# Performance work log

Hardware: AMD Instinct MI355X
Metric: run time of the kernel (lower is better)

Reference implementation:

```python
import jax, jax.numpy as jnp
import numpy as np

N_NODES = 100000
N_REL = 3
N_EDGES = 1600000
IN_F, HID_F, N_CLS = 256, 128, 2


def setup_inputs() -> dict:
    key = jax.random.key(0)
    ks = jax.random.split(key, 6)
    x = jax.random.normal(ks[0], (N_NODES, IN_F), dtype=jnp.float32)
    # edges[r, 0] = src node ids, edges[r, 1] = dst node ids for relation r
    edges = jax.random.randint(ks[1], (N_REL, 2, N_EDGES), 0, N_NODES, dtype=jnp.int64)
    W1 = jax.random.normal(ks[2], (N_REL, IN_F, HID_F), dtype=jnp.float32) * 0.05
    b1 = jnp.zeros((N_REL, HID_F), dtype=jnp.float32)
    W2 = jax.random.normal(ks[3], (N_REL, HID_F, N_CLS), dtype=jnp.float32) * 0.05
    b2 = jnp.zeros((N_REL, N_CLS), dtype=jnp.float32)
    return {"x": x, "edges": edges, "W1": W1, "b1": b1, "W2": W2, "b2": b2}


def _hetero_graphconv(h, edges, W, b, n_nodes):
    """Sum over relations of DGL GraphConv(norm='both', bias=True).
    in_feats > out_feats for every layer here, so (as in DGL) the dense
    transform is applied BEFORE aggregation.
    out_r = D_in^{-1/2} A_r D_out^{-1/2} (h W_r) + b_r
    """
    out = jnp.zeros((n_nodes, W.shape[-1]), dtype=h.dtype)
    ones = jnp.ones((edges.shape[-1],), dtype=h.dtype)
    for r in range(edges.shape[0]):  # small fixed relation count
        src, dst = edges[r, 0], edges[r, 1]
        deg_out = jnp.clip(jax.ops.segment_sum(ones, src, num_segments=n_nodes), 1.0)
        deg_in = jnp.clip(jax.ops.segment_sum(ones, dst, num_segments=n_nodes), 1.0)
        feat = (h * jax.lax.rsqrt(deg_out)[:, None]) @ W[r]          # [N, out]
        agg = jax.ops.segment_sum(feat[src], dst, num_segments=n_nodes)  # scatter-sum
        out = out + agg * jax.lax.rsqrt(deg_in)[:, None] + b[r]
    return out


def reference(x, edges, W1, b1, W2, b2):
    n = x.shape[0]
    h = jax.nn.relu(_hetero_graphconv(x, edges, W1, b1, n))
    return _hetero_graphconv(h, edges, W2, b2, n)
```

## Files before the change

### kernel.cpp

```cpp
#include <hip/hip_runtime.h>
#include <hip/hip_bf16.h>


#define N_REL 3
#define IN_F 256
#define HID_F 128
#define SB_BITS 11
#define SB_SIZE 2048
#define NSBMAX 64
#define TILE 2048

__global__ __launch_bounds__(256) void HeteroGCN_count_kernel(
    const int* __restrict__ edges, unsigned* __restrict__ bcount2,
    int E, int NS) {
  __shared__ unsigned hd[NSBMAX];
  __shared__ unsigned hs[NSBMAX];
  int r = blockIdx.y;
  if (threadIdx.x < NSBMAX) { hd[threadIdx.x] = 0u; hs[threadIdx.x] = 0u; }
  __syncthreads();
  const int* ep = edges + (size_t)r * 2 * E;
  int stride = gridDim.x * 256;
  for (int e = blockIdx.x * 256 + threadIdx.x; e < E; e += stride) {
    int src = ep[e];
    int dst = ep[E + e];
    atomicAdd(&hd[dst >> SB_BITS], 1u);
    atomicAdd(&hs[src >> SB_BITS], 1u);
  }
  __syncthreads();
  if (threadIdx.x < (unsigned)NS) {
    unsigned h = hd[threadIdx.x];
    if (h) atomicAdd(&bcount2[r * NSBMAX + threadIdx.x], h);
    h = hs[threadIdx.x];
    if (h) atomicAdd(&bcount2[(N_REL + r) * NSBMAX + threadIdx.x], h);
  }
}

__global__ __launch_bounds__(64) void HeteroGCN_scan_kernel(
    const unsigned* __restrict__ bcount2, unsigned* __restrict__ sbbase2,
    unsigned* __restrict__ scursor2, int NS) {
  int row = blockIdx.x;
  int t = threadIdx.x;
  unsigned v = (t < NS) ? bcount2[row * NSBMAX + t] : 0u;
  unsigned pre = v;
  #pragma unroll
  for (int d = 1; d < 64; d <<= 1) {
    unsigned tt = __shfl_up(pre, (unsigned)d, 64);
    if (t >= d) pre += tt;
  }
  if (t < NS) {
    sbbase2[row * NSBMAX + t] = pre - v;
    scursor2[row * NSBMAX + t] = pre - v;
  }
}

__global__ __launch_bounds__(256) void HeteroGCN_part_kernel(
    const int* __restrict__ edges, unsigned* __restrict__ scursor2,
    unsigned* __restrict__ staging_dst, unsigned short* __restrict__ staging_src,
    int E, int NS) {
  __shared__ unsigned hd[NSBMAX], hs[NSBMAX];
  __shared__ unsigned toffd[NSBMAX], toffs[NSBMAX];
  __shared__ unsigned gbd[NSBMAX], gbs[NSBMAX];
  __shared__ unsigned ordb[TILE];
  __shared__ unsigned addrb[TILE];
  __shared__ unsigned short srcw[TILE];
  __shared__ unsigned saddr[TILE];
  int r = blockIdx.y;
  const int* ep = edges + (size_t)r * 2 * E;
  int t0 = blockIdx.x * TILE;
  int nt = min(TILE, E - t0);
  if (threadIdx.x < NSBMAX) { hd[threadIdx.x] = 0u; hs[threadIdx.x] = 0u; }
  __syncthreads();
  int sbk[8];
  unsigned rkk[8], pkk[8], rks[8];
  #pragma unroll 8
  for (int k = 0; k < 8; ++k) {
    int ii = k * 256 + (int)threadIdx.x;
    sbk[k] = -1;
    if (ii < nt) {
      int i = t0 + ii;
      int src = ep[i];
      int dst = ep[E + i];
      int sb = dst >> SB_BITS;
      rkk[k] = atomicAdd(&hd[sb], 1u);
      rks[k] = atomicAdd(&hs[src >> SB_BITS], 1u);
      pkk[k] = ((unsigned)src << SB_BITS) | ((unsigned)dst & (SB_SIZE - 1u));
      sbk[k] = sb;
    }
  }
  __syncthreads();
  {
    int w = threadIdx.x >> 6, l = threadIdx.x & 63;
    if (w < 2) {
      unsigned* hh = w ? hs : hd;
      unsigned* tf = w ? toffs : toffd;
      unsigned* gb = w ? gbs : gbd;
      int row = w ? (N_REL + r) : r;
      unsigned v = (l < NS) ? hh[l] : 0u;
      unsigned pre = v;
      #pragma unroll
      for (int d = 1; d < 64; d <<= 1) {
        unsigned tt = __shfl_up(pre, (unsigned)d, 64);
        if (l >= d) pre += tt;
      }
      if (l < NS) {
        tf[l] = pre - v;
        gb[l] = v ? atomicAdd(&scursor2[row * NSBMAX + l], v) : 0u;
      }
    }
  }
  __syncthreads();
  #pragma unroll 8
  for (int k = 0; k < 8; ++k) {
    if (sbk[k] >= 0) {
      unsigned pos = toffd[sbk[k]] + rkk[k];
      ordb[pos] = pkk[k];
      addrb[pos] = gbd[sbk[k]] + rkk[k];
      int sb2 = (int)(pkk[k] >> 22);
      unsigned pos2 = toffs[sb2] + rks[k];
      srcw[pos2] = (unsigned short)((pkk[k] >> SB_BITS) & (SB_SIZE - 1u));
      saddr[pos2] = gbs[sb2] + rks[k];
    }
  }
  __syncthreads();
  unsigned* stg = staging_dst + (size_t)r * E;
  unsigned short* sst = staging_src + (size_t)r * E;
  for (int ii = threadIdx.x; ii < nt; ii += 256) {
    stg[addrb[ii]] = ordb[ii];
    sst[saddr[ii]] = srcw[ii];
  }
}

__global__ __launch_bounds__(256) void HeteroGCN_build_kernel(
    const unsigned* __restrict__ staging_dst, const unsigned* __restrict__ sbbase2,
    const unsigned* __restrict__ bcount2, int* __restrict__ csr_src,
    int* __restrict__ offsets, unsigned* __restrict__ deg_in,
    float* __restrict__ rs_in, int N, int E) {
  __shared__ unsigned hist[SB_SIZE];
  __shared__ unsigned wtot[4];
  int s = blockIdx.x;
  int r = blockIdx.y;
  int tid = threadIdx.x;
  int lane = tid & 63;
  int wid = tid >> 6;
  unsigned base = sbbase2[r * NSBMAX + s];
  unsigned cnt = bcount2[r * NSBMAX + s];
  for (int i = tid; i < SB_SIZE; i += 256) hist[i] = 0u;
  __syncthreads();
  const unsigned* sp = staging_dst + (size_t)r * E + base;
  for (unsigned i = tid; i < cnt; i += 256)
    atomicAdd(&hist[sp[i] & (SB_SIZE - 1u)], 1u);
  __syncthreads();
  unsigned v[8], lsum = 0;
  #pragma unroll 8
  for (int k = 0; k < 8; ++k) {
    v[k] = hist[tid * 8 + k];
    lsum += v[k];
  }
  unsigned pre = lsum;
  #pragma unroll
  for (int d = 1; d < 64; d <<= 1) {
    unsigned tt = __shfl_up(pre, (unsigned)d, 64);
    if (lane >= d) pre += tt;
  }
  if (lane == 63) wtot[wid] = pre;
  __syncthreads();
  unsigned woff = 0;
  for (int w = 0; w < wid; ++w) woff += wtot[w];
  unsigned run = woff + pre - lsum;
  #pragma unroll 8
  for (int k = 0; k < 8; ++k) {
    int node = s * SB_SIZE + tid * 8 + k;
    if (node < N) {
      size_t gi = (size_t)r * N + node;
      deg_in[gi] = v[k];
      rs_in[gi] = rsqrtf((float)max(v[k], 1u));
      offsets[gi] = (int)(base + run);
    }
    hist[tid * 8 + k] = run;
    run += v[k];
  }
  __syncthreads();
  int* cp = csr_src + (size_t)r * E + base;
  for (unsigned i = tid; i < cnt; i += 256) {
    unsigned rec = sp[i];
    unsigned slot = atomicAdd(&hist[rec & (SB_SIZE - 1u)], 1u);
    cp[slot] = (int)(rec >> SB_BITS);
  }
}

__global__ __launch_bounds__(256) void HeteroGCN_degout_kernel(
    const unsigned short* __restrict__ staging_src,
    const unsigned* __restrict__ sbbase2, const unsigned* __restrict__ bcount2,
    float* __restrict__ rs_out, int N, int E) {
  __shared__ unsigned hist[SB_SIZE];
  int s = blockIdx.x;
  int r = blockIdx.y;
  int tid = threadIdx.x;
  unsigned base = sbbase2[(N_REL + r) * NSBMAX + s];
  unsigned cnt = bcount2[(N_REL + r) * NSBMAX + s];
  for (int i = tid; i < SB_SIZE; i += 256) hist[i] = 0u;
  __syncthreads();
  const unsigned short* sp = staging_src + (size_t)r * E + base;
  for (unsigned i = tid; i < cnt; i += 256) atomicAdd(&hist[sp[i]], 1u);
  __syncthreads();
  for (int i = tid; i < SB_SIZE; i += 256) {
    int node = s * SB_SIZE + i;
    if (node < N)
      rs_out[(size_t)r * N + node] = rsqrtf((float)max(hist[i], 1u));
  }
}

__global__ __launch_bounds__(256) void HeteroGCN_gemm1_kernel(
    const float* __restrict__ x, const float* __restrict__ W,
    const float* __restrict__ rs_out, float* __restrict__ feat, int M) {
  __shared__ float As[64][68];
  __shared__ float Bs[64][128];
  int tid = threadIdx.x;
  int block_row = blockIdx.x * 64;
  int rg = tid >> 4;
  int cg = tid & 15;
  int row0 = rg * 4;
  int colA = cg * 4;
  float acc[4][8] = {};
  for (int k0 = 0; k0 < IN_F; k0 += 64) {
    #pragma unroll
    for (int i = 0; i < 4; ++i) {
      int f4 = tid + i * 256;
      int rr = f4 >> 4;
      int cc = (f4 & 15) << 2;
      int grow = block_row + rr;
      float4 vv = make_float4(0.f, 0.f, 0.f, 0.f);
      if (grow < M) vv = *(const float4*)(x + (size_t)grow * IN_F + k0 + cc);
      *(float4*)(&As[rr][cc]) = vv;
    }
    #pragma unroll
    for (int i = 0; i < 8; ++i) {
      int f4 = tid + i * 256;
      int rr = f4 >> 5;
      int cc = (f4 & 31) << 2;
      *(float4*)(&Bs[rr][cc]) = *(const float4*)(W + (size_t)(k0 + rr) * HID_F + cc);
    }
    __syncthreads();
    #pragma unroll
    for (int kk = 0; kk < 64; ++kk) {
      float a[4];
      #pragma unroll
      for (int i = 0; i < 4; ++i) a[i] = As[row0 + i][kk];
      float4 b0 = *(const float4*)(&Bs[kk][colA]);
      float4 b1 = *(const float4*)(&Bs[kk][64 + colA]);
      #pragma unroll
      for (int i = 0; i < 4; ++i) {
        acc[i][0] += a[i] * b0.x; acc[i][1] += a[i] * b0.y;
        acc[i][2] += a[i] * b0.z; acc[i][3] += a[i] * b0.w;
        acc[i][4] += a[i] * b1.x; acc[i][5] += a[i] * b1.y;
        acc[i][6] += a[i] * b1.z; acc[i][7] += a[i] * b1.w;
      }
    }
    __syncthreads();
  }
  #pragma unroll
  for (int i = 0; i < 4; ++i) {
    int grow = block_row + row0 + i;
    if (grow < M) {
      float s = rs_out[grow];
      float4 v0 = make_float4(acc[i][0] * s, acc[i][1] * s, acc[i][2] * s, acc[i][3] * s);
      float4 v1 = make_float4(acc[i][4] * s, acc[i][5] * s, acc[i][6] * s, acc[i][7] * s);
      *(float4*)(feat + (size_t)grow * HID_F + colA) = v0;
      *(float4*)(feat + (size_t)grow * HID_F + 64 + colA) = v1;
    }
  }
}

__global__ __launch_bounds__(256) void HeteroGCN_agg1_kernel(
    const float* __restrict__ feat, const int* __restrict__ csr_r,
    const int* __restrict__ offsets_r, const unsigned* __restrict__ deg_in_r,
    const float* __restrict__ rs_in_r, const float* __restrict__ b1,
    float* __restrict__ h1, int N, int rel) {
  int half = threadIdx.x >> 7;
  int f = threadIdx.x & 127;
  int n = blockIdx.x * 2 + half;
  if (n >= N) return;
  int off = offsets_r[n];
  int cnt = (int)deg_in_r[n];
  const int* sp = csr_r + off;
  float a0 = 0.f, a1 = 0.f, a2 = 0.f, a3 = 0.f;
  int i = 0;
  for (; i + 3 < cnt; i += 4) {
    int s0 = sp[i], s1 = sp[i + 1], s2 = sp[i + 2], s3 = sp[i + 3];
    a0 += feat[(size_t)s0 * HID_F + f];
    a1 += feat[(size_t)s1 * HID_F + f];
    a2 += feat[(size_t)s2 * HID_F + f];
    a3 += feat[(size_t)s3 * HID_F + f];
  }
  for (; i < cnt; ++i) a0 += feat[(size_t)sp[i] * HID_F + f];
  float v = ((a0 + a1) + (a2 + a3)) * rs_in_r[n];
  size_t oi = (size_t)n * HID_F + f;
  if (rel == 0) {
    h1[oi] = v;
  } else if (rel == 1) {
    h1[oi] += v;
  } else {
    float b = b1[f] + b1[HID_F + f] + b1[2 * HID_F + f];
    h1[oi] = fmaxf(h1[oi] + v + b, 0.f);
  }
}

__global__ __launch_bounds__(256) void HeteroGCN_gemm2_kernel(
    const float* __restrict__ h1, const float* __restrict__ W2,
    const float* __restrict__ rs_out, float* __restrict__ feat2, int N) {
  int wid = (blockIdx.x * blockDim.x + threadIdx.x) >> 6;
  int lane = threadIdx.x & 63;
  if (wid >= N) return;
  float2 h = *(const float2*)(h1 + (size_t)wid * HID_F + lane * 2);
  float p[6];
  #pragma unroll
  for (int r = 0; r < 3; ++r) {
    #pragma unroll
    for (int c = 0; c < 2; ++c) {
      float w0 = W2[((size_t)r * HID_F + lane * 2) * 2 + c];
      float w1 = W2[((size_t)r * HID_F + lane * 2 + 1) * 2 + c];
      p[r * 2 + c] = h.x * w0 + h.y * w1;
    }
  }
  #pragma unroll
  for (int o = 32; o > 0; o >>= 1) {
    #pragma unroll
    for (int q = 0; q < 6; ++q) p[q] += __shfl_xor(p[q], o, 64);
  }
  if (lane == 0) {
    #pragma unroll
    for (int q = 0; q < 6; ++q) {
      int r = q >> 1, c = q & 1;
      feat2[((size_t)r * N + wid) * 2 + c] = p[q] * rs_out[r * N + wid];
    }
  }
}

__global__ __launch_bounds__(256) void HeteroGCN_agg2_kernel(
    const float* __restrict__ feat2, const int* __restrict__ csr_src,
    const int* __restrict__ offsets, const unsigned* __restrict__ deg_in,
    const float* __restrict__ rs_in, const float* __restrict__ b2,
    float* __restrict__ out, int N, int E) {
  int n = blockIdx.x * blockDim.x + threadIdx.x;
  if (n >= N) return;
  float o0 = 0.f, o1 = 0.f;
  #pragma unroll
  for (int r = 0; r < 3; ++r) {
    int off = offsets[r * N + n];
    int cnt = (int)deg_in[r * N + n];
    const int* sp = csr_src + (size_t)r * E + off;
    const float* fp = feat2 + (size_t)r * N * 2;
    float a0 = 0.f, a1 = 0.f, c0 = 0.f, c1 = 0.f;
    int i = 0;
    for (; i + 1 < cnt; i += 2) {
      int s0 = sp[i], s1 = sp[i + 1];
      float2 f0 = *(const float2*)(fp + (size_t)s0 * 2);
      float2 f1 = *(const float2*)(fp + (size_t)s1 * 2);
      a0 += f0.x; a1 += f0.y;
      c0 += f1.x; c1 += f1.y;
    }
    if (i < cnt) {
      float2 f0 = *(const float2*)(fp + (size_t)sp[i] * 2);
      a0 += f0.x; a1 += f0.y;
    }
    float ri = rs_in[r * N + n];
    o0 += (a0 + c0) * ri + b2[r * 2 + 0];
    o1 += (a1 + c1) * ri + b2[r * 2 + 1];
  }
  *(float2*)(out + (size_t)n * 2) = make_float2(o0, o1);
}

extern "C" void kernel_launch(void* const* d_in, const int* in_sizes, int n_in,
                              void* d_out, int out_size, void* d_ws, size_t ws_size,
                              hipStream_t stream) {
  const float* x = (const float*)d_in[0];
  const int* edges = (const int*)d_in[1];
  const float* W1 = (const float*)d_in[2];
  const float* b1 = (const float*)d_in[3];
  const float* W2 = (const float*)d_in[4];
  const float* b2 = (const float*)d_in[5];
  float* out = (float*)d_out;

  const int N = in_sizes[0] / IN_F;
  const int E = in_sizes[1] / (N_REL * 2);
  const int NS = (N + SB_SIZE - 1) >> SB_BITS;

  char* ws = (char*)d_ws;
  size_t p = 0;
  auto take = [&](size_t b) { size_t o = p; p += (b + 255) & ~(size_t)255; return o; };
  size_t bcount2_off  = take((size_t)2 * N_REL * NSBMAX * 4);
  size_t sbbase2_off  = take((size_t)2 * N_REL * NSBMAX * 4);
  size_t scursor2_off = take((size_t)2 * N_REL * NSBMAX * 4);
  size_t deg_in_off   = take((size_t)N_REL * N * 4);
  size_t rs_out_off   = take((size_t)N_REL * N * 4);
  size_t rs_in_off    = take((size_t)N_REL * N * 4);
  size_t offsets_off  = take((size_t)N_REL * N * 4);
  size_t csr_off      = take((size_t)N_REL * E * 4);
  size_t feat_off     = take((size_t)N * HID_F * 4);
  size_t h1_off       = take((size_t)N * HID_F * 4);
  size_t feat2_off    = take((size_t)N_REL * N * 2 * 4);
  (void)ws_size;

  unsigned* bcount2  = (unsigned*)(ws + bcount2_off);
  unsigned* sbbase2  = (unsigned*)(ws + sbbase2_off);
  unsigned* scursor2 = (unsigned*)(ws + scursor2_off);
  unsigned* deg_in   = (unsigned*)(ws + deg_in_off);
  float* rs_out = (float*)(ws + rs_out_off);
  float* rs_in  = (float*)(ws + rs_in_off);
  int* offsets  = (int*)(ws + offsets_off);
  int* csr_src  = (int*)(ws + csr_off);
  float* feat   = (float*)(ws + feat_off);
  unsigned* staging_dst = (unsigned*)(ws + feat_off);
  unsigned short* staging_src =
      (unsigned short*)(ws + feat_off + ((size_t)N_REL * E * 4 + 255 & ~(size_t)255));
  float* h1     = (float*)(ws + h1_off);
  float* feat2  = (float*)(ws + feat2_off);

  hipMemsetAsync(ws + bcount2_off, 0, (size_t)2 * N_REL * NSBMAX * 4, stream);

  dim3 blk(256);
  HeteroGCN_count_kernel<<<dim3(512, N_REL), blk, 0, stream>>>(
      edges, bcount2, E, NS);
  HeteroGCN_scan_kernel<<<dim3(2 * N_REL), dim3(64), 0, stream>>>(
      bcount2, sbbase2, scursor2, NS);
  HeteroGCN_part_kernel<<<dim3((E + TILE - 1) / TILE, N_REL), blk, 0, stream>>>(
      edges, scursor2, staging_dst, staging_src, E, NS);
  HeteroGCN_build_kernel<<<dim3(NS, N_REL), blk, 0, stream>>>(
      staging_dst, sbbase2, bcount2, csr_src, offsets, deg_in, rs_in, N, E);
  HeteroGCN_degout_kernel<<<dim3(NS, N_REL), blk, 0, stream>>>(
      staging_src, sbbase2, bcount2, rs_out, N, E);

  for (int r = 0; r < N_REL; ++r) {
    HeteroGCN_gemm1_kernel<<<dim3((N + 63) / 64), blk, 0, stream>>>(
        x, W1 + (size_t)r * IN_F * HID_F, rs_out + (size_t)r * N, feat, N);
    HeteroGCN_agg1_kernel<<<dim3((N + 1) / 2), blk, 0, stream>>>(
        feat, csr_src + (size_t)r * E, offsets + (size_t)r * N,
        deg_in + (size_t)r * N, rs_in + (size_t)r * N, b1, h1, N, r);
  }

  HeteroGCN_gemm2_kernel<<<dim3((N * 64 + 255) / 256), blk, 0, stream>>>(
      h1, W2, rs_out, feat2, N);
  HeteroGCN_agg2_kernel<<<dim3((N + 255) / 256), blk, 0, stream>>>(
      feat2, csr_src, offsets, deg_in, rs_in, b2, out, N, E);
}
```

Measured before the change: 1.112 ms.

## Store layer-1 features in bf16 and fuse three relation aggregations into one kernel

The first-layer GEMM now writes its per-relation features as bf16 into separate buffers, one per relation, instead of reusing a single fp32 buffer. A single aggregation kernel then gathers all three relations per node, with one wave per node and two features per lane, and applies bias and ReLU once. This halves the gather bytes and removes the read-modify-write of h1 across three launches. In exchange it reduces intermediate precision to bf16, which adds rounding error to the sums.

```diff
diff --git a/kernel.cpp b/kernel.cpp
--- a/kernel.cpp
+++ b/kernel.cpp
@@ -9,6 +9,17 @@
 #define SB_SIZE 2048
 #define NSBMAX 64
 #define TILE 2048
+
+__device__ __forceinline__ unsigned short f2bf(float x) {
+  unsigned u = __float_as_uint(x);
+  return (unsigned short)((u + 0x7fffu + ((u >> 16) & 1u)) >> 16);
+}
+__device__ __forceinline__ float2 bf2f(unsigned u) {
+  float2 f;
+  f.x = __uint_as_float(u << 16);
+  f.y = __uint_as_float(u & 0xffff0000u);
+  return f;
+}
 
 __global__ __launch_bounds__(256) void HeteroGCN_count_kernel(
     const int* __restrict__ edges, unsigned* __restrict__ bcount2,
@@ -212,7 +223,7 @@
 
 __global__ __launch_bounds__(256) void HeteroGCN_gemm1_kernel(
     const float* __restrict__ x, const float* __restrict__ W,
-    const float* __restrict__ rs_out, float* __restrict__ feat, int M) {
+    const float* __restrict__ rs_out, unsigned short* __restrict__ feat, int M) {
   __shared__ float As[64][68];
   __shared__ float Bs[64][128];
   int tid = threadIdx.x;
@@ -263,46 +274,66 @@
     int grow = block_row + row0 + i;
     if (grow < M) {
       float s = rs_out[grow];
-      float4 v0 = make_float4(acc[i][0] * s, acc[i][1] * s, acc[i][2] * s, acc[i][3] * s);
-      float4 v1 = make_float4(acc[i][4] * s, acc[i][5] * s, acc[i][6] * s, acc[i][7] * s);
-      *(float4*)(feat + (size_t)grow * HID_F + colA) = v0;
-      *(float4*)(feat + (size_t)grow * HID_F + 64 + colA) = v1;
+      ushort4 v0, v1;
+      v0.x = f2bf(acc[i][0] * s); v0.y = f2bf(acc[i][1] * s);
+      v0.z = f2bf(acc[i][2] * s); v0.w = f2bf(acc[i][3] * s);
+      v1.x = f2bf(acc[i][4] * s); v1.y = f2bf(acc[i][5] * s);
+      v1.z = f2bf(acc[i][6] * s); v1.w = f2bf(acc[i][7] * s);
+      *(ushort4*)(feat + (size_t)grow * HID_F + colA) = v0;
+      *(ushort4*)(feat + (size_t)grow * HID_F + 64 + colA) = v1;
     }
   }
 }
 
 __global__ __launch_bounds__(256) void HeteroGCN_agg1_kernel(
-    const float* __restrict__ feat, const int* __restrict__ csr_r,
-    const int* __restrict__ offsets_r, const unsigned* __restrict__ deg_in_r,
-    const float* __restrict__ rs_in_r, const float* __restrict__ b1,
-    float* __restrict__ h1, int N, int rel) {
-  int half = threadIdx.x >> 7;
-  int f = threadIdx.x & 127;
-  int n = blockIdx.x * 2 + half;
+    const unsigned short* __restrict__ feat0,
+    const unsigned short* __restrict__ feat1,
+    const unsigned short* __restrict__ feat2b,
+    const int* __restrict__ csr, const int* __restrict__ offsets,
+    const unsigned* __restrict__ deg_in, const float* __restrict__ rs_in,
+    const float* __restrict__ b1, float* __restrict__ h1, int N, int E) {
+  int w = threadIdx.x >> 6;
+  int lane = threadIdx.x & 63;
+  int n = blockIdx.x * 4 + w;
   if (n >= N) return;
-  int off = offsets_r[n];
-  int cnt = (int)deg_in_r[n];
-  const int* sp = csr_r + off;
-  float a0 = 0.f, a1 = 0.f, a2 = 0.f, a3 = 0.f;
-  int i = 0;
-  for (; i + 3 < cnt; i += 4) {
-    int s0 = sp[i], s1 = sp[i + 1], s2 = sp[i + 2], s3 = sp[i + 3];
-    a0 += feat[(size_t)s0 * HID_F + f];
-    a1 += feat[(size_t)s1 * HID_F + f];
-    a2 += feat[(size_t)s2 * HID_F + f];
-    a3 += feat[(size_t)s3 * HID_F + f];
-  }
-  for (; i < cnt; ++i) a0 += feat[(size_t)sp[i] * HID_F + f];
-  float v = ((a0 + a1) + (a2 + a3)) * rs_in_r[n];
-  size_t oi = (size_t)n * HID_F + f;
-  if (rel == 0) {
-    h1[oi] = v;
-  } else if (rel == 1) {
-    h1[oi] += v;
-  } else {
-    float b = b1[f] + b1[HID_F + f] + b1[2 * HID_F + f];
-    h1[oi] = fmaxf(h1[oi] + v + b, 0.f);
-  }
+  float hx = 0.f, hy = 0.f;
+  #pragma unroll
+  for (int r = 0; r < 3; ++r) {
+    const unsigned short* fp = (r == 0) ? feat0 : (r == 1) ? feat1 : feat2b;
+    int off = offsets[r * N + n];
+    int cnt = (int)deg_in[r * N + n];
+    const int* sp = csr + (size_t)r * E + off;
+    float a0 = 0.f, a1 = 0.f, b0 = 0.f, bb1 = 0.f;
+    float c0 = 0.f, c1 = 0.f, d0 = 0.f, d1 = 0.f;
+    int i = 0;
+    for (; i + 3 < cnt; i += 4) {
+      int s0 = sp[i], s1 = sp[i + 1], s2 = sp[i + 2], s3 = sp[i + 3];
+      unsigned u0 = *(const unsigned*)(fp + (size_t)s0 * HID_F + lane * 2);
+      unsigned u1 = *(const unsigned*)(fp + (size_t)s1 * HID_F + lane * 2);
+      unsigned u2 = *(const unsigned*)(fp + (size_t)s2 * HID_F + lane * 2);
+      unsigned u3 = *(const unsigned*)(fp + (size_t)s3 * HID_F + lane * 2);
+      float2 v0 = bf2f(u0), v1 = bf2f(u1), v2 = bf2f(u2), v3 = bf2f(u3);
+      a0 += v0.x; a1 += v0.y;
+      b0 += v1.x; bb1 += v1.y;
+      c0 += v2.x; c1 += v2.y;
+      d0 += v3.x; d1 += v3.y;
+    }
+    for (; i < cnt; ++i) {
+      unsigned u = *(const unsigned*)(fp + (size_t)sp[i] * HID_F + lane * 2);
+      float2 v = bf2f(u);
+      a0 += v.x; a1 += v.y;
+    }
+    float ri = rs_in[r * N + n];
+    hx += ((a0 + b0) + (c0 + d0)) * ri;
+    hy += ((a1 + bb1) + (c1 + d1)) * ri;
+  }
+  int f = lane * 2;
+  float bs0 = b1[f] + b1[HID_F + f] + b1[2 * HID_F + f];
+  float bs1 = b1[f + 1] + b1[HID_F + f + 1] + b1[2 * HID_F + f + 1];
+  float2 o;
+  o.x = fmaxf(hx + bs0, 0.f);
+  o.y = fmaxf(hy + bs1, 0.f);
+  *(float2*)(h1 + (size_t)n * HID_F + f) = o;
 }
 
 __global__ __launch_bounds__(256) void HeteroGCN_gemm2_kernel(
@@ -396,7 +427,7 @@
   size_t rs_in_off    = take((size_t)N_REL * N * 4);
   size_t offsets_off  = take((size_t)N_REL * N * 4);
   size_t csr_off      = take((size_t)N_REL * E * 4);
-  size_t feat_off     = take((size_t)N * HID_F * 4);
+  size_t feat3_off    = take((size_t)N_REL * N * HID_F * 2);
   size_t h1_off       = take((size_t)N * HID_F * 4);
   size_t feat2_off    = take((size_t)N_REL * N * 2 * 4);
   (void)ws_size;
@@ -409,10 +440,10 @@
   float* rs_in  = (float*)(ws + rs_in_off);
   int* offsets  = (int*)(ws + offsets_off);
   int* csr_src  = (int*)(ws + csr_off);
-  float* feat   = (float*)(ws + feat_off);
-  unsigned* staging_dst = (unsigned*)(ws + feat_off);
+  unsigned short* feat3 = (unsigned short*)(ws + feat3_off);
+  unsigned* staging_dst = (unsigned*)(ws + feat3_off);
   unsigned short* staging_src =
-      (unsigned short*)(ws + feat_off + ((size_t)N_REL * E * 4 + 255 & ~(size_t)255));
+      (unsigned short*)(ws + feat3_off + (((size_t)N_REL * E * 4 + 255) & ~(size_t)255));
   float* h1     = (float*)(ws + h1_off);
   float* feat2  = (float*)(ws + feat2_off);
 
@@ -432,11 +463,12 @@
 
   for (int r = 0; r < N_REL; ++r) {
     HeteroGCN_gemm1_kernel<<<dim3((N + 63) / 64), blk, 0, stream>>>(
-        x, W1 + (size_t)r * IN_F * HID_F, rs_out + (size_t)r * N, feat, N);
-    HeteroGCN_agg1_kernel<<<dim3((N + 1) / 2), blk, 0, stream>>>(
-        feat, csr_src + (size_t)r * E, offsets + (size_t)r * N,
-        deg_in + (size_t)r * N, rs_in + (size_t)r * N, b1, h1, N, r);
-  }
+        x, W1 + (size_t)r * IN_F * HID_F, rs_out + (size_t)r * N,
+        feat3 + (size_t)r * N * HID_F, N);
+  }
+  HeteroGCN_agg1_kernel<<<dim3((N + 3) / 4), blk, 0, stream>>>(
+      feat3, feat3 + (size_t)N * HID_F, feat3 + (size_t)2 * N * HID_F,
+      csr_src, offsets, deg_in, rs_in, b1, h1, N, E);
 
   HeteroGCN_gemm2_kernel<<<dim3((N * 64 + 255) / 256), blk, 0, stream>>>(
       h1, W2, rs_out, feat2, N);
```

After: 903.3 us. 1.23x faster.
